# Optimization experiments

Hardware: AMD Instinct MI355X
Metric: run time of the kernel (lower is better)

## Reference

```python
import jax, jax.numpy as jnp
import numpy as np

EPS = 1e-12  # torch F.normalize clamp_min eps


def _linear_interp(t, M):
    # PyTorch F.interpolate(mode='linear', align_corners=False) along last axis.
    L = t.shape[-1]
    src = (jnp.arange(M, dtype=t.dtype) + 0.5) * (L / M) - 0.5
    src = jnp.maximum(src, 0.0)
    i0 = jnp.minimum(jnp.floor(src).astype(jnp.int32), L - 1)
    i1 = jnp.minimum(i0 + 1, L - 1)
    frac = src - i0.astype(t.dtype)
    return t[..., i0] * (1.0 - frac) + t[..., i1] * frac


def _l2norm(t):
    n = jnp.linalg.norm(t, axis=-1, keepdims=True)
    return t / jnp.maximum(n, EPS)


def setup_inputs() -> dict:
    key = jax.random.key(0)
    ks = jax.random.split(key, 6)
    b, dim, m = 4, 512, 4096
    h = w = 64
    heads = 8
    s = 0.02
    return {
        "x": jax.random.normal(ks[0], (b, dim, m), dtype=jnp.float32),
        "y": jax.random.normal(ks[1], (b, dim, h, w), dtype=jnp.float32),
        "temperature": jnp.ones((heads, 1, 1), dtype=jnp.float32),
        "w_kv": jax.random.normal(ks[2], (2 * dim, dim), dtype=jnp.float32) * s,
        "w_q": jax.random.normal(ks[3], (dim, dim), dtype=jnp.float32) * s,
        "w_dw": jax.random.normal(ks[4], (dim, dim, 3, 3), dtype=jnp.float32) * s,
        "w_out": jax.random.normal(ks[5], (dim, dim), dtype=jnp.float32) * s,
    }


def reference(x, y, temperature, w_kv, w_q, w_dw, w_out):
    b, c, m = x.shape
    heads = temperature.shape[0]
    hd = c // heads

    # kv = Conv1d(dim, 2*dim, k=1)(x); split into k, v
    kv = jnp.einsum('bcm,oc->bom', x, w_kv)
    k, v = jnp.split(kv, 2, axis=1)

    # q = dwconv3x3(Conv2d 1x1(y)) -> flatten -> linear-resize to m
    q = jnp.einsum('bchw,oc->bohw', y, w_q)
    q = jax.lax.conv_general_dilated(
        q, w_dw, window_strides=(1, 1), padding=[(1, 1), (1, 1)],
        dimension_numbers=('NCHW', 'OIHW', 'NCHW'))
    q = q.reshape(b, c, -1)
    q = _linear_interp(q, m)

    # split heads: [b, head, c', m]
    q = _l2norm(q.reshape(b, heads, hd, m))
    k = _l2norm(k.reshape(b, heads, hd, m))
    v = v.reshape(b, heads, hd, m)

    # channel-wise attention: [b, head, c', c']
    attn = jnp.einsum('bhcm,bhdm->bhcd', q, k) * temperature
    attn = jax.nn.softmax(attn, axis=-1)
    out = jnp.einsum('bhcd,bhdm->bhcm', attn, v).reshape(b, c, m)

    # project_out: Conv1d k=1
    return jnp.einsum('bcm,oc->bom', out, w_out)
```

## Files before the change

### kernel.cpp

```cpp
#include <hip/hip_runtime.h>
#include <hip/hip_bf16.h>
#include <math.h>

typedef float f32x4 __attribute__((ext_vector_type(4)));
typedef int   i32x4 __attribute__((ext_vector_type(4)));
typedef short s16x8 __attribute__((ext_vector_type(8)));

#define NB 4
#define NC 512
#define NM 4096
#define NHEADS 8

#define GLDS16(src, dst) __builtin_amdgcn_global_load_lds( \
    (const __attribute__((address_space(1))) void*)(src),  \
    (__attribute__((address_space(3))) void*)(dst), 16, 0, 0)

__global__ __launch_bounds__(256) void prep(
    const float* __restrict__ wdw, const float* __restrict__ wkv,
    const float* __restrict__ wq,
    __hip_bfloat16* __restrict__ Wr, __hip_bfloat16* __restrict__ wkvB,
    __hip_bfloat16* __restrict__ wqT, __hip_bfloat16* __restrict__ zeropad,
    float* __restrict__ norms)
{
  long idx = (long)blockIdx.x * 256 + threadIdx.x;
  if (idx < 2359296) {
    int r = (int)(idx / 262144);
    int rem = (int)(idx % 262144);
    int o = rem >> 9, i = rem & 511;
    Wr[idx] = __float2bfloat16(wdw[((long)o * 512 + i) * 9 + r]);
  } else if (idx < 2883584) {
    long j = idx - 2359296;
    wkvB[j] = __float2bfloat16(wkv[j]);
  } else if (idx < 3145728) {
    long j = idx - 2883584;
    int c = (int)(j >> 9), cp = (int)(j & 511);
    wqT[j] = __float2bfloat16(wq[(long)cp * 512 + c]);
  } else if (idx < 3145856) {
    zeropad[idx - 3145728] = __float2bfloat16(0.f);
  } else if (idx < 3149952) {
    norms[idx - 3145856] = 0.f;
  }
}

__global__ __launch_bounds__(256) void transpose_k(
    const float* __restrict__ x, const float* __restrict__ y,
    __hip_bfloat16* __restrict__ xT, __hip_bfloat16* __restrict__ yT)
{
  __shared__ __hip_bfloat16 tile[64][68];
  int z = blockIdx.z;
  const float* src = ((z < 4) ? x : y) + (long)(z & 3) * ((long)NC * NM);
  __hip_bfloat16* dst = (z < 4 ? xT : yT) + (long)(z & 3) * ((long)NC * NM);
  int tm = blockIdx.x * 64, tc = blockIdx.y * 64;
  int tx4 = threadIdx.x & 15, trow = threadIdx.x >> 4;
  #pragma unroll
  for (int p = 0; p < 4; p++) {
    int crow = trow + p * 16;
    f32x4 v = *(const f32x4*)&src[(long)(tc + crow) * NM + tm + tx4 * 4];
    #pragma unroll
    for (int t = 0; t < 4; t++) tile[crow][tx4 * 4 + t] = __float2bfloat16(v[t]);
  }
  __syncthreads();
  #pragma unroll
  for (int p = 0; p < 4; p++) {
    int mrow = trow + p * 16;
    union { ushort4 u4; unsigned short u[4]; } o;
    #pragma unroll
    for (int t = 0; t < 4; t++)
      o.u[t] = *(const unsigned short*)&tile[tx4 * 4 + t][mrow];
    *(ushort4*)&dst[(long)(tm + mrow) * NC + tc + tx4 * 4] = o.u4;
  }
}

__global__ __launch_bounds__(256) void gemm_bt(
    const __hip_bfloat16* __restrict__ Aall, long sA,
    const __hip_bfloat16* __restrict__ Ball, long sB,
    __hip_bfloat16* __restrict__ Cball, float* __restrict__ Cfall, long sC,
    int M, int N, int Kd, int outMode)
{
  const __hip_bfloat16* A = Aall + (long)blockIdx.z * sA;
  const __hip_bfloat16* B = Ball + (long)blockIdx.z * sB;
  const int m0 = blockIdx.y * 128, n0 = blockIdx.x * 128;
  __shared__ __hip_bfloat16 As[128 * 32];
  __shared__ __hip_bfloat16 Bs[128 * 32];
  const int tid = threadIdx.x;
  const int wid = tid >> 6, lane = tid & 63;
  const int wm = (wid >> 1) * 64, wn = (wid & 1) * 64;
  const int quad = lane >> 4, l16 = lane & 15;
  const int srow = wid * 32 + (lane >> 2);
  const int scol = (lane & 3) * 8;
  f32x4 acc[4][4] = {};
  for (int k0 = 0; k0 < Kd; k0 += 32) {
    __syncthreads();
    #pragma unroll
    for (int t = 0; t < 2; t++) {
      GLDS16(A + (long)(m0 + srow + t * 16) * Kd + k0 + scol,
             As + (wid * 32 + t * 16) * 32);
      GLDS16(B + (long)(n0 + srow + t * 16) * Kd + k0 + scol,
             Bs + (wid * 32 + t * 16) * 32);
    }
    __builtin_amdgcn_s_waitcnt(0);
    __syncthreads();
    s16x8 bfr[4];
    #pragma unroll
    for (int j = 0; j < 4; j++)
      bfr[j] = *(const s16x8*)(&Bs[(wn + j * 16 + l16) * 32 + quad * 8]);
    #pragma unroll
    for (int i = 0; i < 4; i++) {
      s16x8 af = *(const s16x8*)(&As[(wm + i * 16 + l16) * 32 + quad * 8]);
      #pragma unroll
      for (int j = 0; j < 4; j++)
        acc[i][j] = __builtin_amdgcn_mfma_f32_16x16x32_bf16(af, bfr[j], acc[i][j], 0, 0, 0);
    }
  }
  if (outMode == 1) {
    float* C = Cfall + (long)blockIdx.z * sC;
    #pragma unroll
    for (int i = 0; i < 4; i++)
      #pragma unroll
      for (int j = 0; j < 4; j++) {
        int rbase = m0 + wm + i * 16 + quad * 4;
        int col = n0 + wn + j * 16 + l16;
        #pragma unroll
        for (int r = 0; r < 4; r++)
          C[(long)(rbase + r) * N + col] = acc[i][j][r];
      }
  } else if (outMode == 2) {
    __hip_bfloat16* C = Cball;
    const int rt = blockIdx.z;
    #pragma unroll
    for (int i = 0; i < 4; i++)
      #pragma unroll
      for (int j = 0; j < 4; j++) {
        int obase = m0 + wm + i * 16 + quad * 4;
        int col = n0 + wn + j * 16 + l16;
        #pragma unroll
        for (int r = 0; r < 4; r++) {
          int o = obase + r;
          long idx = ((((long)(rt * 32 + (o >> 4)) * 16 + (col >> 5)) << 9)
                      + ((col >> 3) & 3) * 128 + (o & 15) * 8 + (col & 7));
          C[idx] = __float2bfloat16(acc[i][j][r]);
        }
      }
  } else {
    __hip_bfloat16* C = Cball + (long)blockIdx.z * sC;
    #pragma unroll
    for (int i = 0; i < 4; i++)
      #pragma unroll
      for (int j = 0; j < 4; j++) {
        int rbase = m0 + wm + i * 16 + quad * 4;
        int col = n0 + wn + j * 16 + l16;
        #pragma unroll
        for (int r = 0; r < 4; r++)
          C[(long)(rbase + r) * N + col] = __float2bfloat16(acc[i][j][r]);
      }
  }
}

__global__ __launch_bounds__(256) void gemm_kv(
    const __hip_bfloat16* __restrict__ wkvB,
    const __hip_bfloat16* __restrict__ xT,
    __hip_bfloat16* __restrict__ Kb,
    __hip_bfloat16* __restrict__ Vt,
    float* __restrict__ knorm2)
{
  const int z = blockIdx.z;
  const int b = z & 3;
  const bool kmode = (z < 4);
  const long S = (long)NM * NC;
  const __hip_bfloat16* A = kmode ? wkvB : (xT + b * S);
  const __hip_bfloat16* B = kmode ? (xT + b * S) : (wkvB + 262144);
  __hip_bfloat16* C = kmode ? (Kb + b * S) : (Vt + b * S);
  const int m0 = (kmode ? blockIdx.y : blockIdx.x) * 128;
  const int n0 = (kmode ? blockIdx.x : blockIdx.y) * 128;
  const int N = kmode ? NM : NC;
  __shared__ __hip_bfloat16 As[128 * 32];
  __shared__ __hip_bfloat16 Bs[128 * 32];
  const int tid = threadIdx.x;
  const int wid = tid >> 6, lane = tid & 63;
  const int wm = (wid >> 1) * 64, wn = (wid & 1) * 64;
  const int quad = lane >> 4, l16 = lane & 15;
  const int srow = wid * 32 + (lane >> 2);
  const int scol = (lane & 3) * 8;
  f32x4 acc[4][4] = {};
  for (int k0 = 0; k0 < NC; k0 += 32) {
    __syncthreads();
    #pragma unroll
    for (int t = 0; t < 2; t++) {
      GLDS16(A + (long)(m0 + srow + t * 16) * NC + k0 + scol,
             As + (wid * 32 + t * 16) * 32);
      GLDS16(B + (long)(n0 + srow + t * 16) * NC + k0 + scol,
             Bs + (wid * 32 + t * 16) * 32);
    }
    __builtin_amdgcn_s_waitcnt(0);
    __syncthreads();
    s16x8 bfr[4];
    #pragma unroll
    for (int j = 0; j < 4; j++)
      bfr[j] = *(const s16x8*)(&Bs[(wn + j * 16 + l16) * 32 + quad * 8]);
    #pragma unroll
    for (int i = 0; i < 4; i++) {
      s16x8 af = *(const s16x8*)(&As[(wm + i * 16 + l16) * 32 + quad * 8]);
      #pragma unroll
      for (int j = 0; j < 4; j++)
        acc[i][j] = __builtin_amdgcn_mfma_f32_16x16x32_bf16(af, bfr[j], acc[i][j], 0, 0, 0);
    }
  }
  #pragma unroll
  for (int i = 0; i < 4; i++)
    #pragma unroll
    for (int j = 0; j < 4; j++) {
      int rbase = m0 + wm + i * 16 + quad * 4;
      int col = n0 + wn + j * 16 + l16;
      #pragma unroll
      for (int r = 0; r < 4; r++)
        C[(long)(rbase + r) * N + col] = __float2bfloat16(acc[i][j][r]);
    }
  if (kmode) {
    #pragma unroll
    for (int i = 0; i < 4; i++) {
      int rbase = m0 + wm + i * 16 + quad * 4;
      #pragma unroll
      for (int r = 0; r < 4; r++) {
        float s = 0.f;
        #pragma unroll
        for (int j = 0; j < 4; j++) s += acc[i][j][r] * acc[i][j][r];
        s += __shfl_xor(s, 1); s += __shfl_xor(s, 2);
        s += __shfl_xor(s, 4); s += __shfl_xor(s, 8);
        if (l16 == 0) atomicAdd(&knorm2[b * 512 + rbase + r], s);
      }
    }
  }
}

__global__ __launch_bounds__(256) void conv3x3(
    const __hip_bfloat16* __restrict__ Wp,
    const __hip_bfloat16* __restrict__ yT,
    const __hip_bfloat16* __restrict__ zeropad,
    __hip_bfloat16* __restrict__ q2,
    float* __restrict__ qnorm2)
{
  const int b = blockIdx.z;
  const int n0 = blockIdx.x * 128;
  const int m0 = blockIdx.y * 128;
  __shared__ __hip_bfloat16 As2[2][24 * 512];
  __shared__ __hip_bfloat16 Bs2[2][256 * 32];
  const int tid = threadIdx.x;
  const int wid = tid >> 6, lane = tid & 63;
  const int wm = (wid >> 1) * 64, wn = (wid & 1) * 64;
  const int quad = lane >> 4, l16 = lane & 15;
  const int lrow = lane >> 2;
  const int h0 = n0 >> 6;
  const int mb0b = m0 >> 4;
  const int mwl = wm >> 4;
  const __hip_bfloat16* yb = yT + (long)b * NM * NC;
  f32x4 acc[4][4] = {};
  const s16x8 zero8 = {0, 0, 0, 0, 0, 0, 0, 0};

  const int sq = ((lane & 3) ^ ((lane >> 3) & 3)) * 8;

  int addr0[3][4];
  unsigned vbits = 0;
  #pragma unroll
  for (int t = 0; t < 3; t++) {
    #pragma unroll
    for (int j = 0; j < 4; j++) {
      int nl = wn + j * 16 + l16;
      int wq_ = nl & 63, hr = nl >> 6;
      int wp = wq_ + t - 1;
      unsigned v = ((unsigned)wp) < 64u;
      int p = v ? (hr * 64 + wp) : 0;
      addr0[t][j] = p * 32 + ((quad ^ ((p >> 1) & 3)) * 8);
      vbits |= v << (t * 4 + j);
    }
  }


  #pragma unroll
  for (int k = 0; k < 6; k++) {
    int f = wid * 6 + k;
    GLDS16(Wp + (((long)(((f >> 3)) * 32 + mb0b + (f & 7)) * 16 + 0) << 9) + lane * 8,
           &As2[0][f * 512]);
  }
  #pragma unroll
  for (int t = 0; t < 4; t++) {
    int pr = wid * 64 + t * 16 + lrow;
    int hw = (h0 - 1) * 64 + pr;
    const __hip_bfloat16* src = (((unsigned)hw) < (unsigned)NM)
        ? (yb + (long)hw * NC + sq) : zeropad;
    GLDS16(src, &Bs2[0][(wid * 64 + t * 16) * 32]);
  }
  __builtin_amdgcn_s_waitcnt(0);
  __syncthreads();

  for (int icb = 0; icb < 16; icb++) {
    const __hip_bfloat16* Bcur = &Bs2[icb & 1][0];
    #pragma unroll
    for (int g = 0; g < 3; g++) {
      const int cb = (icb ^ g) & 1;
      const __hip_bfloat16* Acur = &As2[cb][0];
      __hip_bfloat16* Anxt = (__hip_bfloat16*)&As2[cb ^ 1][0];
      if (icb < 15 || g < 2) {
        const int gn = (g == 2) ? 0 : g + 1;
        const int icbn = (g == 2) ? icb + 1 : icb;
        #pragma unroll
        for (int k = 0; k < 6; k++) {
          int f = wid * 6 + k;
          GLDS16(Wp + (((long)((gn * 3 + (f >> 3)) * 32 + mb0b + (f & 7)) * 16 + icbn) << 9) + lane * 8,
                 Anxt + f * 512);
        }
      }
      if (g == 1 && icb < 15) {
        __hip_bfloat16* Bnxt = (__hip_bfloat16*)&Bs2[(icb & 1) ^ 1][0];
        #pragma unroll
        for (int t = 0; t < 4; t++) {
          int pr = wid * 64 + t * 16 + lrow;
          int hw = (h0 - 1) * 64 + pr;
          const __hip_bfloat16* src = (((unsigned)hw) < (unsigned)NM)
              ? (yb + (long)hw * NC + (icb + 1) * 32 + sq) : zeropad;
          GLDS16(src, Bnxt + (wid * 64 + t * 16) * 32);
        }
      }
      #pragma unroll
      for (int t = 0; t < 3; t++) {
        s16x8 bfr[4];
        #pragma unroll
        for (int j = 0; j < 4; j++) {
          s16x8 tt = *(const s16x8*)(&Bcur[addr0[t][j] + g * 2048]);
          bfr[j] = ((vbits >> (t * 4 + j)) & 1u) ? tt : zero8;
        }
        #pragma unroll
        for (int i = 0; i < 4; i++) {
          s16x8 af = *(const s16x8*)(&Acur[(t * 8 + mwl + i) * 512 + lane * 8]);
          #pragma unroll
          for (int j = 0; j < 4; j++)
            acc[i][j] = __builtin_amdgcn_mfma_f32_16x16x32_bf16(af, bfr[j], acc[i][j], 0, 0, 0);
        }
      }
      __builtin_amdgcn_s_waitcnt(0);
      __syncthreads();
    }
  }

  __hip_bfloat16* Cb = q2 + (long)b * NC * NM;
  #pragma unroll
  for (int i = 0; i < 4; i++)
    #pragma unroll
    for (int j = 0; j < 4; j++) {
      int rbase = m0 + wm + i * 16 + quad * 4;
      int col = n0 + wn + j * 16 + l16;
      #pragma unroll
      for (int r = 0; r < 4; r++)
        Cb[(long)(rbase + r) * NM + col] = __float2bfloat16(acc[i][j][r]);
    }
  #pragma unroll
  for (int i = 0; i < 4; i++) {
    int rbase = m0 + wm + i * 16 + quad * 4;
    #pragma unroll
    for (int r = 0; r < 4; r++) {
      float s = 0.f;
      #pragma unroll
      for (int j = 0; j < 4; j++) s += acc[i][j][r] * acc[i][j][r];
      s += __shfl_xor(s, 1); s += __shfl_xor(s, 2);
      s += __shfl_xor(s, 4); s += __shfl_xor(s, 8);
      if (l16 == 0) atomicAdd(&qnorm2[b * 512 + rbase + r], s);
    }
  }
}

__global__ __launch_bounds__(256) void attn_g(
    const __hip_bfloat16* __restrict__ q2, const __hip_bfloat16* __restrict__ Kb,
    float* __restrict__ Gpart)
{
  const int mc = blockIdx.x, h = blockIdx.y, b = blockIdx.z;
  const __hip_bfloat16* qrow = q2 + ((long)b * NC + h * 64) * NM + mc * 512;
  const __hip_bfloat16* krow = Kb + ((long)b * NC + h * 64) * NM + mc * 512;
  __shared__ __hip_bfloat16 Qs[64 * 40];
  __shared__ __hip_bfloat16 Ks[64 * 40];
  const int tid = threadIdx.x;
  const int wid = tid >> 6, lane = tid & 63;
  const int wc = (wid >> 1) * 32, wd = (wid & 1) * 32;
  const int quad = lane >> 4, l16 = lane & 15;
  const int srow = tid >> 2, scol = (tid & 3) * 8;
  f32x4 acc[2][2] = {};
  for (int k0 = 0; k0 < 512; k0 += 32) {
    __syncthreads();
    *(i32x4*)(&Qs[srow * 40 + scol]) = *(const i32x4*)(&qrow[(long)srow * NM + k0 + scol]);
    *(i32x4*)(&Ks[srow * 40 + scol]) = *(const i32x4*)(&krow[(long)srow * NM + k0 + scol]);
    __syncthreads();
    s16x8 bfr[2];
    #pragma unroll
    for (int j = 0; j < 2; j++)
      bfr[j] = *(const s16x8*)(&Ks[(wd + j * 16 + l16) * 40 + quad * 8]);
    #pragma unroll
    for (int i = 0; i < 2; i++) {
      s16x8 af = *(const s16x8*)(&Qs[(wc + i * 16 + l16) * 40 + quad * 8]);
      #pragma unroll
      for (int j = 0; j < 2; j++)
        acc[i][j] = __builtin_amdgcn_mfma_f32_16x16x32_bf16(af, bfr[j], acc[i][j], 0, 0, 0);
    }
  }
  float* gp = Gpart + ((long)((b * 8 + h) * 8 + mc)) * 4096;
  #pragma unroll
  for (int i = 0; i < 2; i++)
    #pragma unroll
    for (int j = 0; j < 2; j++)
      #pragma unroll
      for (int r = 0; r < 4; r++)
        gp[(wc + i * 16 + quad * 4 + r) * 64 + wd + j * 16 + l16] = acc[i][j][r];
}

__global__ __launch_bounds__(256) void softmax_wa(
    const float* __restrict__ Gpart, const float* __restrict__ qnorm2,
    const float* __restrict__ knorm2, const float* __restrict__ temp,
    const float* __restrict__ wout, __hip_bfloat16* __restrict__ Wa)
{
  const int oc = blockIdx.x, h = blockIdx.y, b = blockIdx.z;
  __shared__ float G[64][64];
  __shared__ float Wt[64][65];
  const int tid = threadIdx.x;
  const float tv = temp[h];
  for (int e = tid; e < 4096; e += 256) {
    float s = 0.f;
    #pragma unroll
    for (int p = 0; p < 8; p++)
      s += Gpart[((long)((b * 8 + h) * 8 + p)) * 4096 + e];
    int c = e >> 6, d = e & 63;
    float qn = fmaxf(sqrtf(qnorm2[b * 512 + h * 64 + c]), 1e-12f);
    float kn = fmaxf(sqrtf(knorm2[b * 512 + h * 64 + d]), 1e-12f);
    G[c][d] = s * tv / (qn * kn);
    Wt[c][d] = wout[(long)(oc * 64 + c) * 512 + h * 64 + d];
  }
  __syncthreads();
  int row = tid >> 2, s4 = tid & 3;
  float mx = -1e30f;
  for (int d = s4; d < 64; d += 4) mx = fmaxf(mx, G[row][d]);
  mx = fmaxf(mx, __shfl_xor(mx, 1));
  mx = fmaxf(mx, __shfl_xor(mx, 2));
  float sum = 0.f;
  for (int d = s4; d < 64; d += 4) { float e = __expf(G[row][d] - mx); G[row][d] = e; sum += e; }
  sum += __shfl_xor(sum, 1);
  sum += __shfl_xor(sum, 2);
  float inv = 1.f / sum;
  for (int d = s4; d < 64; d += 4) G[row][d] *= inv;
  __syncthreads();
  int d = tid & 63, og = tid >> 6;
  #pragma unroll
  for (int k2 = 0; k2 < 16; k2++) {
    int o = og * 16 + k2;
    float s = 0.f;
    #pragma unroll 8
    for (int c = 0; c < 64; c++) s += Wt[o][c] * G[c][d];
    Wa[((long)b * 512 + oc * 64 + o) * 512 + h * 64 + d] = __float2bfloat16(s);
  }
}

extern "C" void kernel_launch(void* const* d_in, const int* in_sizes, int n_in,
                              void* d_out, int out_size, void* d_ws, size_t ws_size,
                              hipStream_t stream) {
  const float* x    = (const float*)d_in[0];
  const float* y    = (const float*)d_in[1];
  const float* temp = (const float*)d_in[2];
  const float* wkv  = (const float*)d_in[3];
  const float* wq   = (const float*)d_in[4];
  const float* wdw  = (const float*)d_in[5];
  const float* wout = (const float*)d_in[6];
  float* out = (float*)d_out;

  char* ws = (char*)d_ws;
  const long TEN = 16777216;
  __hip_bfloat16* xT  = (__hip_bfloat16*)(ws);
  __hip_bfloat16* q2  = xT;
  __hip_bfloat16* yT  = (__hip_bfloat16*)(ws + TEN);
  float* Gpart        = (float*)(ws + TEN);
  __hip_bfloat16* Wa  = (__hip_bfloat16*)(ws + TEN + 4718592);
  __hip_bfloat16* Kb  = (__hip_bfloat16*)(ws + 2 * TEN);
  __hip_bfloat16* Vt  = (__hip_bfloat16*)(ws + 3 * TEN);
  __hip_bfloat16* Wfold = (__hip_bfloat16*)(ws + 4 * TEN);
  __hip_bfloat16* Wr    = (__hip_bfloat16*)(ws + 4 * TEN + 4718592);
  __hip_bfloat16* wkvB  = (__hip_bfloat16*)(ws + 4 * TEN + 9437184);
  __hip_bfloat16* wqT   = (__hip_bfloat16*)(ws + 4 * TEN + 10485760);
  __hip_bfloat16* zeropad = (__hip_bfloat16*)(ws + 4 * TEN + 11010048);
  float* norms          = (float*)(ws + 4 * TEN + 11010304);
  float* knorm2 = norms;
  float* qnorm2 = norms + 2048;

  const long S = (long)4096 * 512;
  const long S2 = (long)512 * 512;
  dim3 blk(256);

  prep<<<dim3(12305), blk, 0, stream>>>(wdw, wkv, wq, Wr, wkvB, wqT, zeropad, norms);
  transpose_k<<<dim3(64, 8, 8), blk, 0, stream>>>(x, y, xT, yT);
  gemm_bt<<<dim3(4, 4, 9), blk, 0, stream>>>(Wr, S2, wqT, 0L, Wfold, nullptr, 0L, 512, 512, 512, 2);
  gemm_kv<<<dim3(32, 4, 8), blk, 0, stream>>>(wkvB, xT, Kb, Vt, knorm2);
  conv3x3<<<dim3(32, 4, 4), blk, 0, stream>>>(Wfold, yT, zeropad, q2, qnorm2);
  attn_g<<<dim3(8, 8, 4), blk, 0, stream>>>(q2, Kb, Gpart);
  softmax_wa<<<dim3(8, 8, 4), blk, 0, stream>>>(Gpart, qnorm2, knorm2, temp, wout, Wa);
  gemm_bt<<<dim3(32, 4, 4), blk, 0, stream>>>(Wa, S2, Vt, S, nullptr, out, S, 512, 4096, 512, 1);
  (void)in_sizes; (void)n_in; (void)out_size; (void)ws_size;
}
```

Measured before the change: 300.4 us.

## Coalesce dwconv weight prep, swizzle conv3x3 block order, skip center-tap masking

The prep kernel now has each thread read all nine contiguous taps of one depthwise weight row and write them to the nine planes, which cuts the grid to a third. The conv3x3 kernel remaps its flat block index so that consecutive blocks spread across batch and tile positions, likely to improve L2/XCD locality of shared y and weight tiles. The center-tap column (t=1) drops the per-fragment validity select because that tap is never out of range, which removes some VALU selects from the inner MFMA loop.

```diff
diff --git a/kernel.cpp b/kernel.cpp
--- a/kernel.cpp
+++ b/kernel.cpp
@@ -23,22 +23,22 @@
     float* __restrict__ norms)
 {
   long idx = (long)blockIdx.x * 256 + threadIdx.x;
-  if (idx < 2359296) {
-    int r = (int)(idx / 262144);
-    int rem = (int)(idx % 262144);
-    int o = rem >> 9, i = rem & 511;
-    Wr[idx] = __float2bfloat16(wdw[((long)o * 512 + i) * 9 + r]);
-  } else if (idx < 2883584) {
-    long j = idx - 2359296;
+  if (idx < 262144) {
+    const float* s = wdw + idx * 9;
+    #pragma unroll
+    for (int r = 0; r < 9; r++)
+      Wr[(long)r * 262144 + idx] = __float2bfloat16(s[r]);
+  } else if (idx < 786432) {
+    long j = idx - 262144;
     wkvB[j] = __float2bfloat16(wkv[j]);
-  } else if (idx < 3145728) {
-    long j = idx - 2883584;
+  } else if (idx < 1048576) {
+    long j = idx - 786432;
     int c = (int)(j >> 9), cp = (int)(j & 511);
     wqT[j] = __float2bfloat16(wq[(long)cp * 512 + c]);
-  } else if (idx < 3145856) {
-    zeropad[idx - 3145728] = __float2bfloat16(0.f);
-  } else if (idx < 3149952) {
-    norms[idx - 3145856] = 0.f;
+  } else if (idx < 1048704) {
+    zeropad[idx - 1048576] = __float2bfloat16(0.f);
+  } else if (idx < 1052800) {
+    norms[idx - 1048704] = 0.f;
   }
 }
 
@@ -239,9 +239,11 @@
     __hip_bfloat16* __restrict__ q2,
     float* __restrict__ qnorm2)
 {
-  const int b = blockIdx.z;
-  const int n0 = blockIdx.x * 128;
-  const int m0 = blockIdx.y * 128;
+  const int flat = (int)(blockIdx.x + 32 * blockIdx.y + 128 * blockIdx.z);
+  const int lf = (flat & 7) * 64 + (flat >> 3);
+  const int b = lf >> 7;
+  const int n0 = (lf & 31) * 128;
+  const int m0 = ((lf >> 5) & 3) * 128;
   __shared__ __hip_bfloat16 As2[2][24 * 512];
   __shared__ __hip_bfloat16 Bs2[2][256 * 32];
   const int tid = threadIdx.x;
@@ -274,7 +276,6 @@
     }
   }
 
-
   #pragma unroll
   for (int k = 0; k < 6; k++) {
     int f = wid * 6 + k;
@@ -291,6 +292,34 @@
   }
   __builtin_amdgcn_s_waitcnt(0);
   __syncthreads();
+
+#define TAPSEL(g_, t_) { \
+    s16x8 bfr[4]; \
+    _Pragma("unroll") \
+    for (int j_ = 0; j_ < 4; j_++) { \
+      s16x8 tt = *(const s16x8*)(&Bcur[addr0[t_][j_] + (g_) * 2048]); \
+      bfr[j_] = ((vbits >> ((t_) * 4 + j_)) & 1u) ? tt : zero8; \
+    } \
+    _Pragma("unroll") \
+    for (int i_ = 0; i_ < 4; i_++) { \
+      s16x8 af = *(const s16x8*)(&Acur[((t_) * 8 + mwl + i_) * 512 + lane * 8]); \
+      _Pragma("unroll") \
+      for (int j_ = 0; j_ < 4; j_++) \
+        acc[i_][j_] = __builtin_amdgcn_mfma_f32_16x16x32_bf16(af, bfr[j_], acc[i_][j_], 0, 0, 0); \
+    } }
+
+#define TAPNOSEL(g_, t_) { \
+    s16x8 bfr[4]; \
+    _Pragma("unroll") \
+    for (int j_ = 0; j_ < 4; j_++) \
+      bfr[j_] = *(const s16x8*)(&Bcur[addr0[t_][j_] + (g_) * 2048]); \
+    _Pragma("unroll") \
+    for (int i_ = 0; i_ < 4; i_++) { \
+      s16x8 af = *(const s16x8*)(&Acur[((t_) * 8 + mwl + i_) * 512 + lane * 8]); \
+      _Pragma("unroll") \
+      for (int j_ = 0; j_ < 4; j_++) \
+        acc[i_][j_] = __builtin_amdgcn_mfma_f32_16x16x32_bf16(af, bfr[j_], acc[i_][j_], 0, 0, 0); \
+    } }
 
   for (int icb = 0; icb < 16; icb++) {
     const __hip_bfloat16* Bcur = &Bs2[icb & 1][0];
@@ -320,26 +349,15 @@
           GLDS16(src, Bnxt + (wid * 64 + t * 16) * 32);
         }
       }
-      #pragma unroll
-      for (int t = 0; t < 3; t++) {
-        s16x8 bfr[4];
-        #pragma unroll
-        for (int j = 0; j < 4; j++) {
-          s16x8 tt = *(const s16x8*)(&Bcur[addr0[t][j] + g * 2048]);
-          bfr[j] = ((vbits >> (t * 4 + j)) & 1u) ? tt : zero8;
-        }
-        #pragma unroll
-        for (int i = 0; i < 4; i++) {
-          s16x8 af = *(const s16x8*)(&Acur[(t * 8 + mwl + i) * 512 + lane * 8]);
-          #pragma unroll
-          for (int j = 0; j < 4; j++)
-            acc[i][j] = __builtin_amdgcn_mfma_f32_16x16x32_bf16(af, bfr[j], acc[i][j], 0, 0, 0);
-        }
-      }
+      TAPSEL(g, 0);
+      TAPNOSEL(g, 1);
+      TAPSEL(g, 2);
       __builtin_amdgcn_s_waitcnt(0);
       __syncthreads();
     }
   }
+#undef TAPSEL
+#undef TAPNOSEL
 
   __hip_bfloat16* Cb = q2 + (long)b * NC * NM;
   #pragma unroll
@@ -488,7 +506,7 @@
   const long S2 = (long)512 * 512;
   dim3 blk(256);
 
-  prep<<<dim3(12305), blk, 0, stream>>>(wdw, wkv, wq, Wr, wkvB, wqT, zeropad, norms);
+  prep<<<dim3(4113), blk, 0, stream>>>(wdw, wkv, wq, Wr, wkvB, wqT, zeropad, norms);
   transpose_k<<<dim3(64, 8, 8), blk, 0, stream>>>(x, y, xT, yT);
   gemm_bt<<<dim3(4, 4, 9), blk, 0, stream>>>(Wr, S2, wqT, 0L, Wfold, nullptr, 0L, 512, 512, 512, 2);
   gemm_kv<<<dim3(32, 4, 8), blk, 0, stream>>>(wkvB, xT, Kb, Vt, knorm2);
```

Result: slower. 308.2 us (+2.6%).
